# Performance work log

Measured on AMD Instinct MI355X. Metric: run time of the kernel, lower is better.

The kernel has to match this reference:

```python
import jax, jax.numpy as jnp
import numpy as np

D_MODEL = 1024
N_HEAD = 16
B, T = 2, 2048

def setup_inputs() -> dict:
    key = jax.random.key(0)
    ks = jax.random.split(key, 6)
    s = 0.02
    return {
        "q_raw": jax.random.normal(ks[0], (B, T, D_MODEL), jnp.float32),
        "kv_raw": jax.random.normal(ks[1], (B, T, D_MODEL), jnp.float32),
        "kv_padding_mask": jnp.ones((B, T), jnp.int32),
        "Wq": jax.random.normal(ks[2], (D_MODEL, D_MODEL), jnp.float32) * s,
        "Wk": jax.random.normal(ks[3], (D_MODEL, D_MODEL), jnp.float32) * s,
        "Wv": jax.random.normal(ks[4], (D_MODEL, D_MODEL), jnp.float32) * s,
        "Wo": jax.random.normal(ks[5], (D_MODEL, D_MODEL), jnp.float32) * s,
    }

def reference(q_raw, kv_raw, kv_padding_mask, Wq, Wk, Wv, Wo):
    Bq, Tq, _ = q_raw.shape
    _, Tkv, _ = kv_raw.shape
    dh = D_MODEL // N_HEAD
    # projections (nn.Linear, no bias): x @ W.T
    q = (q_raw @ Wq.T).reshape(Bq, Tq, N_HEAD, dh).transpose(0, 2, 1, 3)   # (B,H,Tq,dh)
    k = (kv_raw @ Wk.T).reshape(Bq, Tkv, N_HEAD, dh).transpose(0, 2, 1, 3)  # (B,H,Tkv,dh)
    v = (kv_raw @ Wv.T).reshape(Bq, Tkv, N_HEAD, dh).transpose(0, 2, 1, 3)
    scores = jnp.einsum('bhqd,bhkd->bhqk', q, k) / jnp.sqrt(jnp.float32(dh))
    neg_inf = jnp.float32(-jnp.inf)
    # causal mask (is_causal_mask=True)
    causal = jnp.tril(jnp.ones((Tq, Tq), jnp.bool_))
    scores = jnp.where(causal[None, None, :, :], scores, neg_inf)
    # kv padding mask: (B,Tkv) -> (B,1,Tq,Tkv)
    pad = (kv_padding_mask != 0)[:, None, None, :]
    scores = jnp.where(pad, scores, neg_inf)
    weights = jax.nn.softmax(scores, axis=-1)
    y = jnp.einsum('bhqk,bhkd->bhqd', weights, v)   # (B,H,Tq,dh)
    # FAITHFUL to original: transpose(2,3) then view(B,Tq,-1)
    y = y.transpose(0, 1, 3, 2).reshape(Bq, Tq, -1)
    return y @ Wo.T
```

## Files before the change

kernel.cpp:

```cpp
#include <hip/hip_runtime.h>

#define B_SZ 2
#define T_SZ 2048
#define DM   1024
#define NH   16
#define DH   64

typedef __attribute__((ext_vector_type(8))) short bf16x8;
typedef __attribute__((ext_vector_type(4))) float f32x4;
typedef __attribute__((ext_vector_type(4))) unsigned int u32x4;
typedef __attribute__((ext_vector_type(4))) unsigned short u16x4;

__device__ __forceinline__ unsigned short f2bf(float f) {
  unsigned u = __builtin_bit_cast(unsigned, f);
  u += 0x7FFFu + ((u >> 16) & 1u);
  return (unsigned short)(u >> 16);
}
__device__ __forceinline__ unsigned packbf(float lo, float hi) {
  return (unsigned)f2bf(lo) | ((unsigned)f2bf(hi) << 16);
}

template<int CTRL>
__device__ __forceinline__ float dpp_mov(float x) {
  return __builtin_bit_cast(float,
      __builtin_amdgcn_update_dpp(0, __builtin_bit_cast(int, x), CTRL, 0xF, 0xF, true));
}
__device__ __forceinline__ float rowsum16(float x) {
  x += dpp_mov<0x128>(x);
  x += dpp_mov<0x124>(x);
  x += dpp_mov<0x122>(x);
  x += dpp_mov<0x121>(x);
  return x;
}

__device__ __forceinline__ void stage16(const float* src, unsigned short* dst) {
  const f32x4* ps = (const f32x4*)src;
  f32x4 v0 = ps[0], v1 = ps[1], v2 = ps[2], v3 = ps[3];
  u32x4 w0, w1;
  w0[0] = packbf(v0[0], v0[1]); w0[1] = packbf(v0[2], v0[3]);
  w0[2] = packbf(v1[0], v1[1]); w0[3] = packbf(v1[2], v1[3]);
  w1[0] = packbf(v2[0], v2[1]); w1[1] = packbf(v2[2], v2[3]);
  w1[2] = packbf(v3[0], v3[1]); w1[3] = packbf(v3[2], v3[3]);
  *(u32x4*)dst = w0;
  *(u32x4*)(dst + 8) = w1;
}

__device__ __forceinline__ void gload16(const unsigned short* g, unsigned short* l) {
  __builtin_amdgcn_global_load_lds(
      (const __attribute__((address_space(1))) unsigned int*)(const void*)g,
      (__attribute__((address_space(3))) unsigned int*)(void*)l, 16, 0, 0);
}

__device__ __forceinline__ void cvt16(const float* s, unsigned short* d, float scale) {
  const f32x4* ps = (const f32x4*)s;
  f32x4 v0 = ps[0] * scale, v1 = ps[1] * scale, v2 = ps[2] * scale, v3 = ps[3] * scale;
  u32x4 w0, w1;
  w0[0] = packbf(v0[0], v0[1]); w0[1] = packbf(v0[2], v0[3]);
  w0[2] = packbf(v1[0], v1[1]); w0[3] = packbf(v1[2], v1[3]);
  w1[0] = packbf(v2[0], v2[1]); w1[1] = packbf(v2[2], v2[3]);
  w1[2] = packbf(v3[0], v3[1]); w1[3] = packbf(v3[2], v3[3]);
  *(u32x4*)d = w0;
  *(u32x4*)(d + 8) = w1;
}

__global__ __launch_bounds__(256) void cvt_all(
    const float* __restrict__ wq, const float* __restrict__ wk,
    const float* __restrict__ wv, const float* __restrict__ wo,
    const float* __restrict__ qr, const float* __restrict__ kvr,
    unsigned short* __restrict__ dq, unsigned short* __restrict__ dk,
    unsigned short* __restrict__ dv, unsigned short* __restrict__ dwo,
    unsigned short* __restrict__ dqr, unsigned short* __restrict__ dkvr,
    float qscale) {
  const int bid = blockIdx.x;
  const float* s; unsigned short* d; float sc = 1.0f; int off;
  if (bid < 1024) {
    const int which = bid >> 8; off = bid & 255;
    s = (which == 0) ? wq : (which == 1) ? wk : (which == 2) ? wv : wo;
    d = (which == 0) ? dq : (which == 1) ? dk : (which == 2) ? dv : dwo;
    if (which == 0) sc = qscale;
  } else {
    const int which = (bid - 1024) >> 10; off = (bid - 1024) & 1023;
    s = which ? kvr : qr;
    d = which ? dkvr : dqr;
  }
  const int i = (off * 256 + threadIdx.x) * 16;
  cvt16(s + i, d + i, sc);
}

__global__ __launch_bounds__(256) void cvt_w4(
    const float* __restrict__ s0, const float* __restrict__ s1,
    const float* __restrict__ s2, const float* __restrict__ s3,
    unsigned short* __restrict__ d0, unsigned short* __restrict__ d1,
    unsigned short* __restrict__ d2, unsigned short* __restrict__ d3,
    float qscale) {
  const int y = blockIdx.y;
  const float* s = (y == 0) ? s0 : (y == 1) ? s1 : (y == 2) ? s2 : s3;
  unsigned short* d = (y == 0) ? d0 : (y == 1) ? d1 : (y == 2) ? d2 : d3;
  const float sc = (y == 0) ? qscale : 1.0f;
  const int i = (blockIdx.x * 256 + threadIdx.x) * 16;
  cvt16(s + i, d + i, sc);
}

template<int AMODE, int BMODE, int CMODE>
__global__ __launch_bounds__(256) void gemm2(
    const void* __restrict__ A0, const void* __restrict__ A1, int lda,
    const void* __restrict__ B0, const void* __restrict__ B1, int ldb, long bZ,
    void* __restrict__ C0, void* __restrict__ C1, int K, int nx, int ny) {
  __shared__ unsigned short As[128 * 32];
  __shared__ unsigned short Bs[64 * 32];
  const int tid = threadIdx.x, lane = tid & 63, w = tid >> 6;
  const int wm = w >> 1, wn = w & 1;
  const int l15 = lane & 15, lg = lane >> 4;

  const int cpx = gridDim.x >> 3;
  const int flat = (blockIdx.x & 7) * cpx + (blockIdx.x >> 3);
  const int nbk = flat % nx;
  const int rest = flat / nx;
  const int mbk = rest % ny;
  const int z = rest / ny;
  const int mblk = mbk * 128, nblk = nbk * 64;

  const void* Ap; const void* Bp; void* Cp;
  long aoff = 0; int zb = 0, zs = 0;
  if constexpr (CMODE == 0) {
    Ap = z ? A1 : A0; Bp = z ? B1 : B0; Cp = z ? C1 : C0;
  } else if constexpr (CMODE == 2) {
    Ap = A0; Cp = C0;
    if constexpr (BMODE == 1) Bp = (const void*)((const unsigned short*)B0 + (long)z * bZ);
    else                      Bp = (const void*)((const float*)B0 + (long)z * bZ);
  } else {
    Ap = A0; Bp = B0; Cp = C0;
    zb = z >> 1; zs = z & 1;
    aoff = (long)zb * 2097152 + (long)zs * 1024;
  }

  f32x4 acc[4][2];
#pragma unroll
  for (int i = 0; i < 4; i++)
#pragma unroll
    for (int j = 0; j < 2; j++) acc[i][j] = (f32x4){0.f, 0.f, 0.f, 0.f};

  const int asr = tid >> 1, asc = (tid & 1) * 16;
  const int agr = w * 32 + (lane >> 2), agc = (lane & 3) * 8;
  const int bgr = w * 16 + (lane >> 2), bgc = (lane & 3) * 8;

  for (int k0 = 0; k0 < K; k0 += 32) {
    if constexpr (AMODE == 0) {
      stage16((const float*)Ap + (long)(mblk + asr) * lda + k0 + asc, &As[asr * 32 + asc]);
    } else {
      const unsigned short* Ab = (const unsigned short*)Ap + aoff;
      gload16(Ab + (long)(mblk + agr) * lda + k0 + agc, &As[w * 1024]);
      gload16(Ab + (long)(mblk + agr + 16) * lda + k0 + agc, &As[w * 1024 + 512]);
    }
    if constexpr (BMODE == 0) {
      if (tid < 128)
        stage16((const float*)Bp + (long)(nblk + asr) * ldb + k0 + asc, &Bs[asr * 32 + asc]);
    } else {
      gload16((const unsigned short*)Bp + (long)(nblk + bgr) * ldb + k0 + bgc, &Bs[w * 512]);
    }
    __syncthreads();

    bf16x8 af[4], bfr[2];
#pragma unroll
    for (int mi = 0; mi < 4; mi++)
      af[mi] = *(const bf16x8*)&As[(wm * 64 + mi * 16 + l15) * 32 + lg * 8];
#pragma unroll
    for (int nj = 0; nj < 2; nj++)
      bfr[nj] = *(const bf16x8*)&Bs[(wn * 32 + nj * 16 + l15) * 32 + lg * 8];
#pragma unroll
    for (int mi = 0; mi < 4; mi++)
#pragma unroll
      for (int nj = 0; nj < 2; nj++)
        acc[mi][nj] = __builtin_amdgcn_mfma_f32_16x16x32_bf16(af[mi], bfr[nj], acc[mi][nj], 0, 0, 0);
    __syncthreads();
  }

#pragma unroll
  for (int mi = 0; mi < 4; mi++) {
#pragma unroll
    for (int nj = 0; nj < 2; nj++) {
#pragma unroll
      for (int r = 0; r < 4; r++) {
        const int i = mblk + wm * 64 + mi * 16 + lg * 4 + r;
        const int n = nblk + wn * 32 + nj * 16 + l15;
        const float v = acc[mi][nj][r];
        if constexpr (CMODE == 0) {
          const int b = i >> 11, t = i & 2047, h = n >> 6, d = n & 63;
          ((unsigned short*)Cp)[((long)(b * NH + h) * T_SZ + t) * DH + d] = f2bf(v);
        } else if constexpr (CMODE == 2) {
          ((unsigned short*)Cp)[(long)z * 2097152 + (long)i * 2048 + n] = f2bf(v);
        } else {
          ((float*)Cp)[(long)zb * T_SZ * DM + (long)(2 * i + zs) * DM + n] = v;
        }
      }
    }
  }
}

__global__ __launch_bounds__(512) void attn3(const unsigned short* __restrict__ Qh,
                                             const unsigned short* __restrict__ Kh,
                                             const unsigned short* __restrict__ Vt,
                                             const int* __restrict__ kmask,
                                             unsigned short* __restrict__ Zt) {
  __shared__ unsigned short lds_kv[2][2][64][72];
  __shared__ unsigned short lds_p[8][16][72];
  __shared__ unsigned long long bmask[32];
  const int tid = threadIdx.x, lane = tid & 63, w = tid >> 6;
  const int l15 = lane & 15, lg = lane >> 4;
  const int g = w >> 2, sw = w & 3;
  const int wg = blockIdx.x;
  const int xcd = wg & 7, lin = wg >> 3;
  const int bh = xcd * 4 + (lin >> 4);
  const int p = lin & 15;
  const int b = bh >> 4, h = bh & 15;
  const int q0a = (31 - p) * 64;
  const int q0b = p * 64;
  const unsigned short* Qb = Qh + ((long)bh << 17);
  const unsigned short* Kb = Kh + ((long)bh << 17);
  const unsigned short* Vtb = Vt + ((long)(b * DM + h * DH)) * T_SZ;
  const long zbase = (long)(b * DM + h * DH) * T_SZ;

#pragma unroll
  for (int k = 0; k < 4; k++) {
    const int ti = w * 4 + k;
    const int mk = kmask[b * T_SZ + ti * 64 + lane];
    const unsigned long long bm = __ballot(mk != 0);
    if (lane == 0) bmask[ti] = bm;
  }

  int q0 = g ? q0b : q0a;
  bf16x8 qf0, qf1;
  {
    const int qra = q0 + sw * 16 + l15;
    qf0 = *(const bf16x8*)(Qb + ((long)qra << 6) + lg * 8);
    qf1 = *(const bf16x8*)(Qb + ((long)qra << 6) + 32 + lg * 8);
  }
  int qc0 = q0 + sw * 16 + lg * 4;

  f32x4 o[4];
  float lr[4];
#pragma unroll
  for (int i = 0; i < 4; i++) {
    o[i] = (f32x4){0.f, 0.f, 0.f, 0.f};
    lr[i] = 0.f;
  }

  const int quarter = tid >> 7, sg = quarter >> 1, skv = quarter & 1;
  const int srow = (tid & 127) >> 1;
  const int soff = (tid & 1) * 32;
  const unsigned short* kp = Kb + ((long)srow << 6) + soff;
  const unsigned short* vp = Vtb + (long)srow * T_SZ + soff;

  u32x4 pr0, pr1, pr2, pr3;
  auto issue = [&](int it) {
    int j0s;
    if (sg == 0) j0s = it * 64;
    else j0s = (it <= p) ? it * 64 : ((it < 16) ? (16 + it - p) * 64 : 0);
    const u32x4* s = (const u32x4*)(skv ? (vp + j0s) : (kp + ((long)j0s << 6)));
    pr0 = s[0]; pr1 = s[1]; pr2 = s[2]; pr3 = s[3];
  };

  auto writeZ = [&](const f32x4* oo, const float* ll, int qq) {
    float inv[4];
#pragma unroll
    for (int r = 0; r < 4; r++) inv[r] = (ll[r] > 0.f) ? (1.f / ll[r]) : 0.f;
#pragma unroll
    for (int nb = 0; nb < 4; nb++) {
      u16x4 pk;
#pragma unroll
      for (int r = 0; r < 4; r++) pk[r] = f2bf(oo[nb][r] * inv[r]);
      *(u16x4*)&Zt[zbase + (long)(nb * 16 + l15) * T_SZ + qq] = pk;
    }
  };

  issue(0);
  for (int it = 0; it < 17; ++it) {
    __syncthreads();
    *(u32x4*)&lds_kv[sg][skv][srow][soff] = pr0;
    *(u32x4*)&lds_kv[sg][skv][srow][soff + 8] = pr1;
    *(u32x4*)&lds_kv[sg][skv][srow][soff + 16] = pr2;
    *(u32x4*)&lds_kv[sg][skv][srow][soff + 24] = pr3;
    __syncthreads();
    if (it + 1 < 17) issue(it + 1);

    if (g == 1 && it == p + 1) {
      writeZ(o, lr, qc0);
#pragma unroll
      for (int i = 0; i < 4; i++) {
        o[i] = (f32x4){0.f, 0.f, 0.f, 0.f};
        lr[i] = 0.f;
      }
      q0 = q0a;
      const int qra = q0 + sw * 16 + l15;
      qf0 = *(const bf16x8*)(Qb + ((long)qra << 6) + lg * 8);
      qf1 = *(const bf16x8*)(Qb + ((long)qra << 6) + 32 + lg * 8);
      qc0 = q0 + sw * 16 + lg * 4;
    }

    int j0 = it * 64;
    bool valid = true;
    if (g == 1) {
      if (it <= p) j0 = it * 64;
      else if (it < 16) j0 = (16 + it - p) * 64;
      else valid = false;
    }

    if (valid) {
      const unsigned long long kvm = bmask[j0 >> 6];

      f32x4 sa[4];
      __builtin_amdgcn_s_setprio(1);
#pragma unroll
      for (int cb = 0; cb < 4; cb++) {
        bf16x8 kf0 = *(const bf16x8*)&lds_kv[g][0][cb * 16 + l15][lg * 8];
        bf16x8 kf1 = *(const bf16x8*)&lds_kv[g][0][cb * 16 + l15][32 + lg * 8];
        f32x4 t = {0.f, 0.f, 0.f, 0.f};
        t = __builtin_amdgcn_mfma_f32_16x16x32_bf16(qf0, kf0, t, 0, 0, 0);
        t = __builtin_amdgcn_mfma_f32_16x16x32_bf16(qf1, kf1, t, 0, 0, 0);
        sa[cb] = t;
      }
      __builtin_amdgcn_s_setprio(0);

      const bool diag = (j0 == q0);
      if (diag || kvm != ~0ull) {
#pragma unroll
        for (int cb = 0; cb < 4; cb++) {
          const int kk = cb * 16 + l15;
          const bool mk2 = (kvm >> kk) & 1ull;
#pragma unroll
          for (int r = 0; r < 4; r++) {
            const bool ok = mk2 && (!diag || (j0 + kk <= qc0 + r));
            sa[cb][r] = ok ? sa[cb][r] : -1e30f;
          }
        }
      }
#pragma unroll
      for (int r = 0; r < 4; r++) {
        float ts = 0.f;
#pragma unroll
        for (int cb = 0; cb < 4; cb++) {
          const float pe = __builtin_amdgcn_exp2f(sa[cb][r]);
          sa[cb][r] = pe;
          ts += pe;
        }
        lr[r] += rowsum16(ts);
      }

#pragma unroll
      for (int cb = 0; cb < 4; cb++)
#pragma unroll
        for (int r = 0; r < 4; r++)
          lds_p[w][lg * 4 + r][cb * 16 + l15] = f2bf(sa[cb][r]);
      bf16x8 pf0 = *(const bf16x8*)&lds_p[w][l15][lg * 8];
      bf16x8 pf1 = *(const bf16x8*)&lds_p[w][l15][32 + lg * 8];

      __builtin_amdgcn_s_setprio(1);
#pragma unroll
      for (int nb = 0; nb < 4; nb++) {
        bf16x8 vf0 = *(const bf16x8*)&lds_kv[g][1][nb * 16 + l15][lg * 8];
        bf16x8 vf1 = *(const bf16x8*)&lds_kv[g][1][nb * 16 + l15][32 + lg * 8];
        f32x4 t = o[nb];
        t = __builtin_amdgcn_mfma_f32_16x16x32_bf16(pf0, vf0, t, 0, 0, 0);
        t = __builtin_amdgcn_mfma_f32_16x16x32_bf16(pf1, vf1, t, 0, 0, 0);
        o[nb] = t;
      }
      __builtin_amdgcn_s_setprio(0);
    }
  }

  __syncthreads();
  float* obuf = (float*)&lds_kv[0][0][0][0];
  float* mlb  = obuf + 4 * 16 * 65;
  if (g == 1) {
#pragma unroll
    for (int nb = 0; nb < 4; nb++)
#pragma unroll
      for (int r = 0; r < 4; r++)
        obuf[(sw * 16 + lg * 4 + r) * 65 + nb * 16 + l15] = o[nb][r];
    if (l15 == 0) {
#pragma unroll
      for (int r = 0; r < 4; r++)
        mlb[sw * 16 + lg * 4 + r] = lr[r];
    }
  }
  __syncthreads();
  if (g == 0) {
    float inv[4];
#pragma unroll
    for (int r = 0; r < 4; r++) {
      const float ls = lr[r] + mlb[sw * 16 + lg * 4 + r];
      inv[r] = (ls > 0.f) ? (1.f / ls) : 0.f;
    }
#pragma unroll
    for (int nb = 0; nb < 4; nb++) {
      u16x4 pk;
#pragma unroll
      for (int r = 0; r < 4; r++) {
        const float o1 = obuf[(sw * 16 + lg * 4 + r) * 65 + nb * 16 + l15];
        pk[r] = f2bf((o[nb][r] + o1) * inv[r]);
      }
      *(u16x4*)&Zt[zbase + (long)(nb * 16 + l15) * T_SZ + qc0] = pk;
    }
  }
}

extern "C" void kernel_launch(void* const* d_in, const int* in_sizes, int n_in,
                              void* d_out, int out_size, void* d_ws, size_t ws_size,
                              hipStream_t stream) {
  const float* q_raw  = (const float*)d_in[0];
  const float* kv_raw = (const float*)d_in[1];
  const int*   kmask  = (const int*)d_in[2];
  const float* Wq = (const float*)d_in[3];
  const float* Wk = (const float*)d_in[4];
  const float* Wv = (const float*)d_in[5];
  const float* Wo = (const float*)d_in[6];
  float* out = (float*)d_out;

  const float QSCALE = 0.125f * 1.44269504088896f;

  unsigned short* ws = (unsigned short*)d_ws;
  unsigned short* Qh = ws;
  unsigned short* Kh = ws + 4194304;
  unsigned short* Vt = ws + 8388608;
  unsigned short* Zt = ws + 12582912;
  const bool full = ws_size >= (size_t)58720256;

  if (full) {
    unsigned short* wqb = ws + 16777216;
    unsigned short* wkb = ws + 17825792;
    unsigned short* wvb = ws + 18874368;
    unsigned short* wob = ws + 19922944;
    unsigned short* qb  = ws + 20971520;
    unsigned short* kvb = ws + 25165824;
    cvt_all<<<dim3(3072), 256, 0, stream>>>(Wq, Wk, Wv, Wo, q_raw, kv_raw,
                                            wqb, wkb, wvb, wob, qb, kvb, QSCALE);
    gemm2<1, 1, 0><<<dim3(1024), 256, 0, stream>>>(
        qb, kvb, DM, wqb, wkb, DM, 0L, Qh, Kh, DM, 16, 32);
    gemm2<1, 1, 2><<<dim3(512), 256, 0, stream>>>(
        wvb, nullptr, DM, kvb, nullptr, DM, 2097152L, Vt, nullptr, DM, 32, 8);
    attn3<<<dim3(512), 512, 0, stream>>>(Qh, Kh, Vt, kmask, Zt);
    gemm2<1, 1, 1><<<dim3(512), 256, 0, stream>>>(
        Zt, nullptr, T_SZ, wob, nullptr, DM, 0L, out, nullptr, DM, 16, 8);
  } else {
    unsigned short* wqb = ws + 12582912;
    unsigned short* wkb = ws + 13631488;
    unsigned short* wvb = ws + 14680064;
    cvt_w4<<<dim3(256, 3), 256, 0, stream>>>(Wq, Wk, Wv, Wv, wqb, wkb, wvb, wvb, QSCALE);
    gemm2<0, 1, 0><<<dim3(1024), 256, 0, stream>>>(
        q_raw, kv_raw, DM, wqb, wkb, DM, 0L, Qh, Kh, DM, 16, 32);
    gemm2<1, 0, 2><<<dim3(512), 256, 0, stream>>>(
        wvb, nullptr, DM, kv_raw, nullptr, DM, 2097152L, Vt, nullptr, DM, 32, 8);
    attn3<<<dim3(512), 512, 0, stream>>>(Qh, Kh, Vt, kmask, Zt);
    gemm2<1, 0, 1><<<dim3(512), 256, 0, stream>>>(
        Zt, nullptr, T_SZ, Wo, nullptr, DM, 0L, out, nullptr, DM, 16, 8);
  }
}
```

Before: 127.4 us.

## Fuse Q/K/V projection launches and compute softmax row sums via MFMA

Merges the Q/K projection GEMM and the V-transpose GEMM into one launch of 1536 blocks, which removes a kernel launch and the tail of the first GEMM. In the attention kernel, the DPP row-sum reduction is replaced by two extra MFMAs that multiply P by a ones vector. P is also converted to bf16 by truncation instead of round-to-nearest. The changes trade fewer VALU/DPP ops for extra MFMA work, and truncation adds a small numeric bias.

```diff
diff --git a/kernel.cpp b/kernel.cpp
--- a/kernel.cpp
+++ b/kernel.cpp
@@ -18,19 +18,6 @@
 }
 __device__ __forceinline__ unsigned packbf(float lo, float hi) {
   return (unsigned)f2bf(lo) | ((unsigned)f2bf(hi) << 16);
-}
-
-template<int CTRL>
-__device__ __forceinline__ float dpp_mov(float x) {
-  return __builtin_bit_cast(float,
-      __builtin_amdgcn_update_dpp(0, __builtin_bit_cast(int, x), CTRL, 0xF, 0xF, true));
-}
-__device__ __forceinline__ float rowsum16(float x) {
-  x += dpp_mov<0x128>(x);
-  x += dpp_mov<0x124>(x);
-  x += dpp_mov<0x122>(x);
-  x += dpp_mov<0x121>(x);
-  return x;
 }
 
 __device__ __forceinline__ void stage16(const float* src, unsigned short* dst) {
@@ -191,6 +178,87 @@
           ((unsigned short*)Cp)[(long)z * 2097152 + (long)i * 2048 + n] = f2bf(v);
         } else {
           ((float*)Cp)[(long)zb * T_SZ * DM + (long)(2 * i + zs) * DM + n] = v;
+        }
+      }
+    }
+  }
+}
+
+__global__ __launch_bounds__(256) void gemm_qkvt(
+    const unsigned short* __restrict__ qb, const unsigned short* __restrict__ kvb,
+    const unsigned short* __restrict__ wqb, const unsigned short* __restrict__ wkb,
+    const unsigned short* __restrict__ wvb,
+    unsigned short* __restrict__ Qh, unsigned short* __restrict__ Kh,
+    unsigned short* __restrict__ Vt) {
+  __shared__ unsigned short As[128 * 32];
+  __shared__ unsigned short Bs[64 * 32];
+  const int tid = threadIdx.x, lane = tid & 63, w = tid >> 6;
+  const int wm = w >> 1, wn = w & 1;
+  const int l15 = lane & 15, lg = lane >> 4;
+
+  const int cpx = gridDim.x >> 3;
+  const int flat = (blockIdx.x & 7) * cpx + (blockIdx.x >> 3);
+
+  const unsigned short* Ap; const unsigned short* Bp;
+  int mblk, nblk, z, mode;
+  if (flat < 1024) {
+    const int nbk = flat % 16; const int rest = flat / 16;
+    const int mbk = rest % 32; z = rest / 32;
+    mblk = mbk * 128; nblk = nbk * 64;
+    Ap = z ? kvb : qb; Bp = z ? wkb : wqb; mode = 0;
+  } else {
+    const int f2 = flat - 1024;
+    const int nbk = f2 % 32; const int rest = f2 / 32;
+    const int mbk = rest % 8; z = rest / 8;
+    mblk = mbk * 128; nblk = nbk * 64;
+    Ap = wvb; Bp = kvb + (long)z * 2097152; mode = 1;
+  }
+
+  f32x4 acc[4][2];
+#pragma unroll
+  for (int i = 0; i < 4; i++)
+#pragma unroll
+    for (int j = 0; j < 2; j++) acc[i][j] = (f32x4){0.f, 0.f, 0.f, 0.f};
+
+  const int agr = w * 32 + (lane >> 2), agc = (lane & 3) * 8;
+  const int bgr = w * 16 + (lane >> 2), bgc = (lane & 3) * 8;
+
+  for (int k0 = 0; k0 < DM; k0 += 32) {
+    gload16(Ap + (long)(mblk + agr) * DM + k0 + agc, &As[w * 1024]);
+    gload16(Ap + (long)(mblk + agr + 16) * DM + k0 + agc, &As[w * 1024 + 512]);
+    gload16(Bp + (long)(nblk + bgr) * DM + k0 + bgc, &Bs[w * 512]);
+    __syncthreads();
+
+    bf16x8 af[4], bfr[2];
+#pragma unroll
+    for (int mi = 0; mi < 4; mi++)
+      af[mi] = *(const bf16x8*)&As[(wm * 64 + mi * 16 + l15) * 32 + lg * 8];
+#pragma unroll
+    for (int nj = 0; nj < 2; nj++)
+      bfr[nj] = *(const bf16x8*)&Bs[(wn * 32 + nj * 16 + l15) * 32 + lg * 8];
+#pragma unroll
+    for (int mi = 0; mi < 4; mi++)
+#pragma unroll
+      for (int nj = 0; nj < 2; nj++)
+        acc[mi][nj] = __builtin_amdgcn_mfma_f32_16x16x32_bf16(af[mi], bfr[nj], acc[mi][nj], 0, 0, 0);
+    __syncthreads();
+  }
+
+  unsigned short* Cp = (mode == 0) ? (z ? Kh : Qh) : Vt;
+#pragma unroll
+  for (int mi = 0; mi < 4; mi++) {
+#pragma unroll
+    for (int nj = 0; nj < 2; nj++) {
+#pragma unroll
+      for (int r = 0; r < 4; r++) {
+        const int i = mblk + wm * 64 + mi * 16 + lg * 4 + r;
+        const int n = nblk + wn * 32 + nj * 16 + l15;
+        const float v = acc[mi][nj][r];
+        if (mode == 0) {
+          const int b = i >> 11, t = i & 2047, h = n >> 6, d = n & 63;
+          Cp[((long)(b * NH + h) * T_SZ + t) * DH + d] = f2bf(v);
+        } else {
+          Cp[(long)z * 2097152 + (long)i * 2048 + n] = f2bf(v);
         }
       }
     }
@@ -220,6 +288,8 @@
   const unsigned short* Vtb = Vt + ((long)(b * DM + h * DH)) * T_SZ;
   const long zbase = (long)(b * DM + h * DH) * T_SZ;
 
+  const bf16x8 ones = {0x3F80, 0x3F80, 0x3F80, 0x3F80, 0x3F80, 0x3F80, 0x3F80, 0x3F80};
+
 #pragma unroll
   for (int k = 0; k < 4; k++) {
     const int ti = w * 4 + k;
@@ -335,26 +405,20 @@
         }
       }
 #pragma unroll
-      for (int r = 0; r < 4; r++) {
-        float ts = 0.f;
-#pragma unroll
-        for (int cb = 0; cb < 4; cb++) {
+      for (int cb = 0; cb < 4; cb++)
+#pragma unroll
+        for (int r = 0; r < 4; r++) {
           const float pe = __builtin_amdgcn_exp2f(sa[cb][r]);
-          sa[cb][r] = pe;
-          ts += pe;
+          lds_p[w][lg * 4 + r][cb * 16 + l15] =
+              (unsigned short)(__builtin_bit_cast(unsigned, pe) >> 16);
         }
-        lr[r] += rowsum16(ts);
-      }
-
-#pragma unroll
-      for (int cb = 0; cb < 4; cb++)
-#pragma unroll
-        for (int r = 0; r < 4; r++)
-          lds_p[w][lg * 4 + r][cb * 16 + l15] = f2bf(sa[cb][r]);
       bf16x8 pf0 = *(const bf16x8*)&lds_p[w][l15][lg * 8];
       bf16x8 pf1 = *(const bf16x8*)&lds_p[w][l15][32 + lg * 8];
 
       __builtin_amdgcn_s_setprio(1);
+      f32x4 ls = {0.f, 0.f, 0.f, 0.f};
+      ls = __builtin_amdgcn_mfma_f32_16x16x32_bf16(pf0, ones, ls, 0, 0, 0);
+      ls = __builtin_amdgcn_mfma_f32_16x16x32_bf16(pf1, ones, ls, 0, 0, 0);
 #pragma unroll
       for (int nb = 0; nb < 4; nb++) {
         bf16x8 vf0 = *(const bf16x8*)&lds_kv[g][1][nb * 16 + l15][lg * 8];
@@ -365,6 +429,8 @@
         o[nb] = t;
       }
       __builtin_amdgcn_s_setprio(0);
+#pragma unroll
+      for (int r = 0; r < 4; r++) lr[r] += ls[r];
     }
   }
 
@@ -388,8 +454,8 @@
     float inv[4];
 #pragma unroll
     for (int r = 0; r < 4; r++) {
-      const float ls = lr[r] + mlb[sw * 16 + lg * 4 + r];
-      inv[r] = (ls > 0.f) ? (1.f / ls) : 0.f;
+      const float ls2 = lr[r] + mlb[sw * 16 + lg * 4 + r];
+      inv[r] = (ls2 > 0.f) ? (1.f / ls2) : 0.f;
     }
 #pragma unroll
     for (int nb = 0; nb < 4; nb++) {
@@ -434,10 +500,7 @@
     unsigned short* kvb = ws + 25165824;
     cvt_all<<<dim3(3072), 256, 0, stream>>>(Wq, Wk, Wv, Wo, q_raw, kv_raw,
                                             wqb, wkb, wvb, wob, qb, kvb, QSCALE);
-    gemm2<1, 1, 0><<<dim3(1024), 256, 0, stream>>>(
-        qb, kvb, DM, wqb, wkb, DM, 0L, Qh, Kh, DM, 16, 32);
-    gemm2<1, 1, 2><<<dim3(512), 256, 0, stream>>>(
-        wvb, nullptr, DM, kvb, nullptr, DM, 2097152L, Vt, nullptr, DM, 32, 8);
+    gemm_qkvt<<<dim3(1536), 256, 0, stream>>>(qb, kvb, wqb, wkb, wvb, Qh, Kh, Vt);
     attn3<<<dim3(512), 512, 0, stream>>>(Qh, Kh, Vt, kmask, Zt);
     gemm2<1, 1, 1><<<dim3(512), 256, 0, stream>>>(
         Zt, nullptr, T_SZ, wob, nullptr, DM, 0L, out, nullptr, DM, 16, 8);
```

New measurement: 122.4 us. 3.9% less time.
